# Performance work log

Hardware: AMD Instinct MI355X
Metric: run time of the kernel (lower is better)

## Reference

```python
import jax, jax.numpy as jnp
import numpy as np

WAVE_LEN = 1000.0

def rank_embedding(rank_dim, feat_dim):
    half = feat_dim // 2
    dim_mat = jnp.arange(half, dtype=jnp.float32) / half
    inv = 1.0 / jnp.power(WAVE_LEN, dim_mat)            # [half]
    mul = jnp.arange(rank_dim, dtype=jnp.float32)[:, None] * inv[None, :]  # [K, half]
    return jnp.concatenate([jnp.sin(mul), jnp.cos(mul)], axis=-1)          # [K, feat_dim]

def setup_inputs() -> dict:
    key = jax.random.key(0)
    ks = jax.random.split(key, 16)
    K, NS, NC, D, DF, H, DK = 2048, 18, 19, 1024, 128, 16, 64
    s = 0.02
    return {
        "size_scores": jax.random.normal(ks[0], (1, K, NS), jnp.float32),
        "size_residuals_normalized": jax.random.normal(ks[1], (1, K, NS, 3), jnp.float32),
        "sem_cls_scores": jax.random.normal(ks[2], (K, NC), jnp.float32),
        "appearance_features": jax.random.normal(ks[3], (K, D), jnp.float32),
        "mean_size_arr": jax.random.uniform(ks[4], (NS, 3), jnp.float32, 0.1, 1.0),
        "w_rank": jax.random.normal(ks[5], (D, DF), jnp.float32) * s,
        "b_rank": jnp.zeros((DF,), jnp.float32),
        "w_roi": jax.random.normal(ks[6], (D, DF), jnp.float32) * s,
        "b_roi": jnp.zeros((DF,), jnp.float32),
        "Wq": jax.random.normal(ks[7], (H, DF, DK), jnp.float32) * s,
        "Wk": jax.random.normal(ks[8], (H, DF, DK), jnp.float32) * s,
        "Wv": jax.random.normal(ks[9], (H, D, DK), jnp.float32) * s,
        "w_logit": jax.random.normal(ks[10], (D, 1), jnp.float32) * s,
        "b_logit": jnp.zeros((1,), jnp.float32),
    }

def reference(size_scores, size_residuals_normalized, sem_cls_scores,
              appearance_features, mean_size_arr,
              w_rank, b_rank, w_roi, b_roi, Wq, Wk, Wv, w_logit, b_logit):
    K, D = appearance_features.shape
    # --- predicted box size: gather residual for argmax size class ---
    pred_size_class = jnp.argmax(size_scores, axis=-1)                     # [1,K]
    size_residuals = size_residuals_normalized * mean_size_arr[None, None] # [1,K,NS,3]
    pred_size_residual = jnp.take_along_axis(
        size_residuals, pred_size_class[..., None, None], axis=2)[:, :, 0, :]  # [1,K,3]
    psc = pred_size_class[0]                                               # [K]
    box_size = mean_size_arr[psc] + pred_size_residual[0]                  # [K,3]
    # --- semantic class prob ---
    prob_all = jax.nn.softmax(sem_cls_scores, axis=-1)                     # [K,NC]
    prob = jnp.max(prob_all, axis=-1)                                      # [K]
    prob_argmax = jnp.argmax(prob_all, axis=-1)                            # [K]
    cls_bbox = box_size                                                    # [K,3]
    # --- background masking (jit-friendly analog of nonzero filtering):
    # background (class 0) proposals get key -1 so they sort to the end with score 0.
    fg = prob_argmax > 0
    sort_key = jnp.where(fg, prob, -1.0)
    order = jnp.argsort(-sort_key)                                         # descending
    sorted_prob = jnp.where(fg[order], prob[order], 0.0)                   # [K]
    sorted_labels = prob_argmax[order]                                     # [K]
    sorted_cls_bboxes = cls_bbox[order]                                    # [K,3]
    sorted_features = appearance_features[order]                           # [K,D]
    # --- rank embedding + roi embedding ---
    emb = rank_embedding(K, D)                                             # [K,D]
    nms_rank = emb @ w_rank + b_rank                                       # [K,DF]
    roi = sorted_features @ w_roi + b_roi                                  # [K,DF]
    e = nms_rank + roi                                                     # [K,DF]
    # --- relation-module self-attention: Q/K from embedding, V from features ---
    dk = Wq.shape[-1]
    q = jnp.einsum('kd,hde->hke', e, Wq)                                   # [H,K,dk]
    k = jnp.einsum('kd,hde->hke', e, Wk)
    scores = jnp.einsum('hke,hme->hkm', q, k) / jnp.sqrt(jnp.float32(dk))  # [H,K,K]
    attn = jax.nn.softmax(scores, axis=-1)
    v = jnp.einsum('kf,hfe->hke', sorted_features, Wv)                     # [H,K,dk]
    o = jnp.einsum('hkm,hme->hke', attn, v)                                # [H,K,dk]
    o = jnp.transpose(o, (1, 0, 2)).reshape(K, -1)                         # [K,D]
    attn_out = sorted_features + o                                         # residual
    # --- nms logit ---
    logit = attn_out @ w_logit + b_logit                                   # [K,1]
    s1 = jax.nn.sigmoid(logit).reshape(-1)
    nms_scores = s1 * sorted_prob
    return nms_scores, sorted_labels - 1, sorted_cls_bboxes
```

## Files before the change

kernel.cpp:

```cpp
#include <hip/hip_runtime.h>

#define KP 2048
#define DD 1024
#define DF 128
#define NH 16
#define DKK 64
#define NSS 18
#define NCC 19
#define NCH 4
#define CHUNK 512

typedef __attribute__((ext_vector_type(8))) short short8;
typedef __attribute__((ext_vector_type(4))) short short4_t;
typedef __attribute__((ext_vector_type(4))) float f32x4;

__device__ __forceinline__ short f2bf(float x){
    unsigned u = __float_as_uint(x);
    u += 0x7fffu + ((u >> 16) & 1u);
    return (short)(u >> 16);
}
__device__ __forceinline__ float bf2f(short s){
    return __uint_as_float(((unsigned)(unsigned short)s) << 16);
}

__device__ __forceinline__ void gl2lds16(const void* g, void* l){
    __builtin_amdgcn_global_load_lds((const __attribute__((address_space(1))) void*)g,
                                     (__attribute__((address_space(3))) void*)l, 16, 0, 0);
}

__global__ void prep_kernel(const float* __restrict__ size_scores,
                            const float* __restrict__ srn,
                            const float* __restrict__ sem,
                            const float* __restrict__ mean,
                            float* __restrict__ box, int* __restrict__ label,
                            double* __restrict__ probd, double* __restrict__ keyd){
    int k = blockIdx.x * blockDim.x + threadIdx.x;
    if (k >= KP) return;
    const float* ss = size_scores + k * NSS;
    int psc = 0; float bs = ss[0];
    for (int s = 1; s < NSS; s++){ float v = ss[s]; if (v > bs){ bs = v; psc = s; } }
    for (int c = 0; c < 3; c++){
        float m = mean[psc * 3 + c];
        float r = srn[k * (NSS * 3) + psc * 3 + c];
        box[k * 3 + c] = m + r * m;
    }
    const float* cs = sem + k * NCC;
    double mx = (double)cs[0]; int lab = 0;
    for (int c = 1; c < NCC; c++){ double v = (double)cs[c]; if (v > mx){ mx = v; lab = c; } }
    double sum = 0.0;
    for (int c = 0; c < NCC; c++) sum += exp((double)cs[c] - mx);
    double prob = 1.0 / sum;
    probd[k] = prob;
    label[k] = lab;
    keyd[k]  = (lab > 0) ? prob : -1.0;
}

__global__ __launch_bounds__(256) void rank_kernel(const double* __restrict__ keyd,
                                                   const int* __restrict__ label,
                                                   const double* __restrict__ probd,
                                                   const float* __restrict__ box,
                                                   int* __restrict__ order, float* __restrict__ sprob,
                                                   float* __restrict__ out){
    int i = blockIdx.x, t = threadIdx.x;
    double ki = keyd[i];
    const double2* k2 = (const double2*)keyd;
    int r = 0;
    #pragma unroll
    for (int p = 0; p < KP / 2 / 256; p++){
        int idx2 = p * 256 + t;
        double2 kj = k2[idx2];
        int j0 = idx2 * 2;
        r += (int)(kj.x > ki) + (int)((kj.x == ki) & (j0 < i));
        r += (int)(kj.y > ki) + (int)((kj.y == ki) & (j0 + 1 < i));
    }
    #pragma unroll
    for (int off = 32; off > 0; off >>= 1) r += __shfl_down(r, off);
    __shared__ int red[4];
    if ((t & 63) == 0) red[t >> 6] = r;
    __syncthreads();
    if (t == 0){
        int rk = red[0] + red[1] + red[2] + red[3];
        order[rk] = i;
        sprob[rk] = (label[i] > 0) ? (float)probd[i] : 0.f;
        out[KP + rk] = (float)(label[i] - 1);
        out[2 * KP + 3 * rk + 0] = box[i * 3 + 0];
        out[2 * KP + 3 * rk + 1] = box[i * 3 + 1];
        out[2 * KP + 3 * rk + 2] = box[i * 3 + 2];
    }
}

__global__ __launch_bounds__(256) void af_kernel(const float* __restrict__ app,
                                                 const int* __restrict__ order,
                                                 short* __restrict__ af){
    int pos = blockIdx.x, t = threadIdx.x;
    int ord = order[pos];
    float4 v = ((const float4*)(app + (size_t)ord * DD))[t];
    short4_t g = { f2bf(v.x), f2bf(v.y), f2bf(v.z), f2bf(v.w) };
    *(short4_t*)(af + (size_t)pos * 2048 + 1024 + t * 4) = g;
    short4_t e;
    #pragma unroll
    for (int i = 0; i < 4; i++){
        int j = t * 4 + i, jj = j & 511;
        float inv = exp2f(-(float)jj * 0.0194644224310197f);
        float arg = (float)pos * inv;
        e[i] = f2bf((j < 512) ? __sinf(arg) : __cosf(arg));
    }
    *(short4_t*)(af + (size_t)pos * 2048 + t * 4) = e;
}

__global__ __launch_bounds__(256) void convw_kernel(const float* __restrict__ w_rank,
                                                    const float* __restrict__ w_roi,
                                                    const float* __restrict__ Wq,
                                                    const float* __restrict__ Wk,
                                                    const float* __restrict__ Wv,
                                                    short* __restrict__ wcat,
                                                    short* __restrict__ qkT,
                                                    short* __restrict__ bvT){
    __shared__ float tile[64][65];
    int b = blockIdx.x;
    const float* src; short* dst; int sstride, dstride, r0, c0, doff;
    float scale = 1.0f;
    if (b < 32){        src = w_rank; dst = wcat; sstride = DF; dstride = 2048;
                        r0 = (b >> 1) * 64; c0 = (b & 1) * 64; doff = 0; }
    else if (b < 64){   int i = b - 32; src = w_roi; dst = wcat; sstride = DF; dstride = 2048;
                        r0 = (i >> 1) * 64; c0 = (i & 1) * 64; doff = 1024; }
    else if (b < 96){   int i = b - 64; int h = i >> 1;
                        src = Wq + (size_t)h * DF * DKK; dst = qkT + (size_t)h * DKK * DF;
                        sstride = DKK; dstride = DF; r0 = (i & 1) * 64; c0 = 0; doff = 0;
                        scale = 0.125f; }
    else if (b < 128){  int i = b - 96; int h = i >> 1;
                        src = Wk + (size_t)h * DF * DKK; dst = qkT + (size_t)(1024 + h * DKK) * DF;
                        sstride = DKK; dstride = DF; r0 = (i & 1) * 64; c0 = 0; doff = 0; }
    else {              int i = b - 128; int h = i >> 4;
                        src = Wv + (size_t)h * DD * DKK; dst = bvT + (size_t)h * DKK * DD;
                        sstride = DKK; dstride = DD; r0 = (i & 15) * 64; c0 = 0; doff = 0; }
    int tx = threadIdx.x & 63, ty = threadIdx.x >> 6;
    #pragma unroll
    for (int p = 0; p < 16; p++){
        int r = p * 4 + ty;
        tile[r][tx] = src[(size_t)(r0 + r) * sstride + c0 + tx];
    }
    __syncthreads();
    #pragma unroll
    for (int p = 0; p < 16; p++){
        int r = p * 4 + ty;
        dst[(size_t)(c0 + r) * dstride + doff + r0 + tx] = f2bf(tile[tx][r] * scale);
    }
}

__global__ __launch_bounds__(256) void gemm_lds(const short* __restrict__ A,
                                                const short* __restrict__ BT,
                                                void* __restrict__ C,
                                                int lda, int ldb, int N,
                                                int klen, size_t slabstride, int mode){
    int w = threadIdx.x >> 6, lane = threadIdx.x & 63;
    int quad = lane >> 4, l16 = lane & 15;
    int m0 = blockIdx.x * 64, n0 = blockIdx.y * 64;
    int kb = blockIdx.z * klen;

    __shared__ __align__(16) short alds[64 * 64];
    __shared__ __align__(16) short blds[64 * 64];

    int p0 = w * 64 + lane;
    int r0 = p0 >> 3, q0 = ((p0 & 7) ^ (r0 & 7)) * 8;
    int p1 = p0 + 256;
    int r1 = p1 >> 3, q1 = ((p1 & 7) ^ (r1 & 7)) * 8;
    short* adst0 = alds + w * 512;
    short* adst1 = alds + 2048 + w * 512;
    short* bdst0 = blds + w * 512;
    short* bdst1 = blds + 2048 + w * 512;
    const short* asrc0 = A + (size_t)(m0 + r0) * lda + kb + q0;
    const short* asrc1 = A + (size_t)(m0 + r1) * lda + kb + q1;
    const short* bsrc0 = BT + (size_t)(n0 + r0) * ldb + kb + q0;
    const short* bsrc1 = BT + (size_t)(n0 + r1) * ldb + kb + q1;

    f32x4 acc[4];
    for (int c = 0; c < 4; c++) acc[c] = (f32x4){0.f, 0.f, 0.f, 0.f};

    for (int kt = 0; kt < klen; kt += 64){
        __syncthreads();
        gl2lds16(asrc0 + kt, adst0);
        gl2lds16(asrc1 + kt, adst1);
        gl2lds16(bsrc0 + kt, bdst0);
        gl2lds16(bsrc1 + kt, bdst1);
        __syncthreads();
        int arow = w * 16 + l16;
        #pragma unroll
        for (int s = 0; s < 2; s++){
            short8 a = *(const short8*)(alds + arow * 64 + (((s * 4 + quad) ^ (l16 & 7)) * 8));
            #pragma unroll
            for (int c = 0; c < 4; c++){
                int brow = c * 16 + l16;
                short8 b = *(const short8*)(blds + brow * 64 + (((s * 4 + quad) ^ (l16 & 7)) * 8));
                acc[c] = __builtin_amdgcn_mfma_f32_16x16x32_bf16(a, b, acc[c], 0, 0, 0);
            }
        }
    }
    int mrow = m0 + w * 16 + quad * 4;
    #pragma unroll
    for (int c = 0; c < 4; c++){
        #pragma unroll
        for (int r = 0; r < 4; r++){
            size_t idx = (size_t)(mrow + r) * N + n0 + c * 16 + l16;
            if (mode == 2) ((short*)C)[idx] = f2bf(acc[c][r]);
            else ((float*)C + (size_t)blockIdx.z * slabstride)[idx] = acc[c][r];
        }
    }
}

__global__ __launch_bounds__(256) void combine_e_kernel(const float* __restrict__ es,
                                                        const float* __restrict__ b_rank,
                                                        const float* __restrict__ b_roi,
                                                        short* __restrict__ e_bf){
    int tid = blockIdx.x * 256 + threadIdx.x;
    int base = tid * 4;
    int n = base & (DF - 1);
    float4 s = *(const float4*)(es + base);
    #pragma unroll
    for (int c = 1; c < 4; c++){
        float4 t = *(const float4*)(es + (size_t)c * KP * DF + base);
        s.x += t.x; s.y += t.y; s.z += t.z; s.w += t.w;
    }
    float4 br = *(const float4*)(b_rank + n);
    float4 bo = *(const float4*)(b_roi + n);
    short4_t o = { f2bf(s.x + br.x + bo.x), f2bf(s.y + br.y + bo.y),
                   f2bf(s.z + br.z + bo.z), f2bf(s.w + br.w + bo.w) };
    *(short4_t*)(e_bf + base) = o;
}

__global__ __launch_bounds__(256, 4) void attn_kernel(const short* __restrict__ qk,
                                                      const short* __restrict__ vt_bf,
                                                      short* __restrict__ po,
                                                      float* __restrict__ pl){
    int qt = blockIdx.x, h = blockIdx.y, ch = blockIdx.z;
    int tid = threadIdx.x;
    int w = tid >> 6, lane = tid & 63, quad = lane >> 4, l16 = lane & 15;
    int qb = qt * 128;

    __shared__ __align__(16) short klds[64 * 64];
    __shared__ __align__(16) short vlds[64 * 64];
    __shared__ short plds[4][16 * 72];
    short* pw = plds[w];

    short8 aq[2][2];
    #pragma unroll
    for (int t = 0; t < 2; t++){
        const short* qrow = qk + (size_t)(qb + t * 64 + w * 16 + l16) * 2048 + h * DKK;
        aq[t][0] = *(const short8*)(qrow + quad * 8);
        aq[t][1] = *(const short8*)(qrow + 32 + quad * 8);
    }

    f32x4 oacc[2][4];
    float lpart[2][4];
    #pragma unroll
    for (int t = 0; t < 2; t++)
        #pragma unroll
        for (int c = 0; c < 4; c++){
            oacc[t][c] = (f32x4){0.f, 0.f, 0.f, 0.f};
            lpart[t][c] = 0.f;
        }

    int seg0 = w * 128 + lane;
    int row0 = seg0 >> 3, c80 = (seg0 & 7) ^ (row0 & 7);
    int seg1 = seg0 + 64;
    int row1 = seg1 >> 3, c81 = (seg1 & 7) ^ (row1 & 7);
    short* kl0 = klds + (size_t)(w * 128) * 8;
    short* kl1 = klds + (size_t)(w * 128 + 64) * 8;
    short* vl0 = vlds + (size_t)(w * 128) * 8;
    short* vl1 = vlds + (size_t)(w * 128 + 64) * 8;

    for (int m0 = ch * CHUNK; m0 < (ch + 1) * CHUNK; m0 += 64){
        __syncthreads();
        gl2lds16(qk + (size_t)(m0 + row0) * 2048 + 1024 + h * DKK + c80 * 8, kl0);
        gl2lds16(qk + (size_t)(m0 + row1) * 2048 + 1024 + h * DKK + c81 * 8, kl1);
        gl2lds16(vt_bf + (size_t)(h * DKK + row0) * KP + m0 + c80 * 8, vl0);
        gl2lds16(vt_bf + (size_t)(h * DKK + row1) * KP + m0 + c81 * 8, vl1);
        __syncthreads();

        #pragma unroll
        for (int t = 0; t < 2; t++){
            f32x4 s[4];
            #pragma unroll
            for (int c = 0; c < 4; c++){
                int r = c * 16 + l16, sw = r & 7;
                short8 b0 = *(const short8*)(klds + r * 64 + (quad ^ sw) * 8);
                short8 b1 = *(const short8*)(klds + r * 64 + ((quad + 4) ^ sw) * 8);
                f32x4 acc = (f32x4){0.f, 0.f, 0.f, 0.f};
                acc = __builtin_amdgcn_mfma_f32_16x16x32_bf16(aq[t][0], b0, acc, 0, 0, 0);
                acc = __builtin_amdgcn_mfma_f32_16x16x32_bf16(aq[t][1], b1, acc, 0, 0, 0);
                #pragma unroll
                for (int rr = 0; rr < 4; rr++) s[c][rr] = __expf(acc[rr]);
            }
            #pragma unroll
            for (int c = 0; c < 4; c++)
                #pragma unroll
                for (int rr = 0; rr < 4; rr++){
                    lpart[t][rr] += s[c][rr];
                    pw[(quad * 4 + rr) * 72 + c * 16 + l16] = f2bf(s[c][rr]);
                }
            short8 pa0 = *(const short8*)(pw + l16 * 72 + quad * 8);
            short8 pa1 = *(const short8*)(pw + l16 * 72 + 32 + quad * 8);
            #pragma unroll
            for (int c = 0; c < 4; c++){
                int r = c * 16 + l16, sw = r & 7;
                short8 bv0 = *(const short8*)(vlds + r * 64 + (quad ^ sw) * 8);
                short8 bv1 = *(const short8*)(vlds + r * 64 + ((quad + 4) ^ sw) * 8);
                oacc[t][c] = __builtin_amdgcn_mfma_f32_16x16x32_bf16(pa0, bv0, oacc[t][c], 0, 0, 0);
                oacc[t][c] = __builtin_amdgcn_mfma_f32_16x16x32_bf16(pa1, bv1, oacc[t][c], 0, 0, 0);
            }
        }
    }

    #pragma unroll
    for (int t = 0; t < 2; t++){
        #pragma unroll
        for (int rr = 0; rr < 4; rr++){
            float v = lpart[t][rr];
            v += __shfl_xor(v, 1); v += __shfl_xor(v, 2);
            v += __shfl_xor(v, 4); v += __shfl_xor(v, 8);
            lpart[t][rr] = v;
        }
        int qr0 = qb + t * 64 + w * 16;
        if (l16 == 0){
            #pragma unroll
            for (int rr = 0; rr < 4; rr++)
                pl[((size_t)ch * NH + h) * KP + qr0 + quad * 4 + rr] = lpart[t][rr];
        }
        #pragma unroll
        for (int c = 0; c < 4; c++)
            #pragma unroll
            for (int rr = 0; rr < 4; rr++)
                po[(size_t)ch * KP * DD + (size_t)(qr0 + quad * 4 + rr) * DD + h * DKK + c * 16 + l16]
                    = f2bf(oacc[t][c][rr]);
    }
}

__global__ __launch_bounds__(256) void final_kernel(const float* __restrict__ app,
                                                    const int* __restrict__ order,
                                                    const short* __restrict__ po,
                                                    const float* __restrict__ pl,
                                                    const float* __restrict__ w_logit,
                                                    const float* __restrict__ b_logit,
                                                    const float* __restrict__ sprob,
                                                    float* __restrict__ out){
    int pos = blockIdx.x, t = threadIdx.x;
    int ord = order[pos];
    int d = t * 4;
    int h = d >> 6;
    float l = 0.f;
    #pragma unroll
    for (int c = 0; c < NCH; c++) l += pl[((size_t)c * NH + h) * KP + pos];
    float inv = 1.f / l;
    float sx = 0, sy = 0, sz = 0, sw = 0;
    #pragma unroll
    for (int c = 0; c < NCH; c++){
        short4_t p = *(const short4_t*)(po + (size_t)c * KP * DD + (size_t)pos * DD + d);
        sx += bf2f(p[0]); sy += bf2f(p[1]); sz += bf2f(p[2]); sw += bf2f(p[3]);
    }
    float4 a = *(const float4*)(app + (size_t)ord * DD + d);
    float4 wv = *(const float4*)(w_logit + d);
    float partial = (a.x + sx * inv) * wv.x + (a.y + sy * inv) * wv.y +
                    (a.z + sz * inv) * wv.z + (a.w + sw * inv) * wv.w;
    for (int off = 32; off > 0; off >>= 1) partial += __shfl_down(partial, off);
    __shared__ float red[4];
    if ((t & 63) == 0) red[t >> 6] = partial;
    __syncthreads();
    if (t == 0){
        float logit = red[0] + red[1] + red[2] + red[3] + b_logit[0];
        float s1 = 1.f / (1.f + __expf(-logit));
        out[pos] = s1 * sprob[pos];
    }
}

extern "C" void kernel_launch(void* const* d_in, const int* in_sizes, int n_in,
                              void* d_out, int out_size, void* d_ws, size_t ws_size,
                              hipStream_t stream){
    (void)in_sizes; (void)n_in; (void)out_size; (void)ws_size;
    const float* size_scores = (const float*)d_in[0];
    const float* srn     = (const float*)d_in[1];
    const float* sem     = (const float*)d_in[2];
    const float* app     = (const float*)d_in[3];
    const float* mean    = (const float*)d_in[4];
    const float* w_rank  = (const float*)d_in[5];
    const float* b_rank  = (const float*)d_in[6];
    const float* w_roi   = (const float*)d_in[7];
    const float* b_roi   = (const float*)d_in[8];
    const float* Wq      = (const float*)d_in[9];
    const float* Wk      = (const float*)d_in[10];
    const float* Wv      = (const float*)d_in[11];
    const float* w_logit = (const float*)d_in[12];
    const float* b_logit = (const float*)d_in[13];
    float* out = (float*)d_out;

    char* ws = (char*)d_ws;
    size_t off = 0;
    auto alloc = [&](size_t n) -> char* {
        char* p = ws + off;
        off = (off + n + 255) & ~(size_t)255;
        return p;
    };
    float*  box    = (float*) alloc((size_t)KP * 3 * 4);
    int*    label  = (int*)   alloc((size_t)KP * 4);
    double* probd  = (double*)alloc((size_t)KP * 8);
    double* keyd   = (double*)alloc((size_t)KP * 8);
    int*    order  = (int*)   alloc((size_t)KP * 4);
    float*  sprob  = (float*) alloc((size_t)KP * 4);
    short*  wcat   = (short*) alloc((size_t)DF * 2048 * 2);
    short*  qkT    = (short*) alloc((size_t)2048 * DF * 2);
    short*  bvT    = (short*) alloc((size_t)DD * DD * 2);
    short*  e_bf   = (short*) alloc((size_t)KP * DF * 2);
    short*  qk_bf  = (short*) alloc((size_t)KP * 2048 * 2);
    short*  vt_bf  = (short*) alloc((size_t)DD * KP * 2);
    float*  pl     = (float*) alloc((size_t)NCH * NH * KP * 4);
    char*   X      = alloc((size_t)NCH * KP * DD * 2);
    short*  af     = (short*)X;
    float*  es     = (float*)(X + (size_t)8 * 1024 * 1024);
    short*  po     = (short*)X;

    prep_kernel<<<KP / 256, 256, 0, stream>>>(size_scores, srn, sem, mean, box, label, probd, keyd);
    rank_kernel<<<KP, 256, 0, stream>>>(keyd, label, probd, box, order, sprob, out);
    af_kernel<<<KP, 256, 0, stream>>>(app, order, af);
    convw_kernel<<<384, 256, 0, stream>>>(w_rank, w_roi, Wq, Wk, Wv, wcat, qkT, bvT);
    gemm_lds<<<dim3(KP / 64, DF / 64, 4), 256, 0, stream>>>(af, wcat, es, 2048, 2048, DF, 512,
                                                            (size_t)KP * DF, 0);
    combine_e_kernel<<<(KP * DF / 4) / 256, 256, 0, stream>>>(es, b_rank, b_roi, e_bf);
    gemm_lds<<<dim3(KP / 64, 2048 / 64, 1), 256, 0, stream>>>(e_bf, qkT, qk_bf, DF, DF, 2048, DF,
                                                              0, 2);
    gemm_lds<<<dim3(DD / 64, KP / 64, 1), 256, 0, stream>>>(bvT, af + 1024, vt_bf, DD, 2048, KP, DD,
                                                            0, 2);
    attn_kernel<<<dim3(KP / 128, NH, NCH), 256, 0, stream>>>(qk_bf, vt_bf, po, pl);
    final_kernel<<<KP, 256, 0, stream>>>(app, order, po, pl, w_logit, b_logit, sprob, out);
}
```

Baseline: 170.6 us.

## Fold logit projection into V so attention reduces to weighted scalar sums

Only the logit (attn_out @ w_logit) is consumed downstream, so w_logit is folded into Wv per head to give a 1024x16 projection. The per-key scalar values are then computed with a small MFMA kernel. Attention now accumulates only exp-sums and exp-weighted scalar sums instead of the full PV MFMA with a 64-wide V tile. This drops the large V GEMM, the V LDS staging, the bf16 partial-output writes and their readback in the final kernel, at the cost of slight numeric reordering and bf16 rounding of the folded weights.

```diff
diff --git a/kernel.cpp b/kernel.cpp
--- a/kernel.cpp
+++ b/kernel.cpp
@@ -18,9 +18,6 @@
     unsigned u = __float_as_uint(x);
     u += 0x7fffu + ((u >> 16) & 1u);
     return (short)(u >> 16);
-}
-__device__ __forceinline__ float bf2f(short s){
-    return __uint_as_float(((unsigned)(unsigned short)s) << 16);
 }
 
 __device__ __forceinline__ void gl2lds16(const void* g, void* l){
@@ -113,11 +110,24 @@
                                                     const float* __restrict__ Wq,
                                                     const float* __restrict__ Wk,
                                                     const float* __restrict__ Wv,
+                                                    const float* __restrict__ w_logit,
                                                     short* __restrict__ wcat,
                                                     short* __restrict__ qkT,
-                                                    short* __restrict__ bvT){
+                                                    short* __restrict__ uT){
+    int b = blockIdx.x;
+    if (b >= 128){
+        int i = b - 128;
+        int h = i >> 2;
+        int f = ((i & 3) << 8) + threadIdx.x;
+        const float* wv = Wv + (size_t)h * DD * DKK + (size_t)f * DKK;
+        const float* wlh = w_logit + h * DKK;
+        float s = 0.f;
+        #pragma unroll
+        for (int e = 0; e < DKK; e++) s += wv[e] * wlh[e];
+        uT[h * DD + f] = f2bf(s);
+        return;
+    }
     __shared__ float tile[64][65];
-    int b = blockIdx.x;
     const float* src; short* dst; int sstride, dstride, r0, c0, doff;
     float scale = 1.0f;
     if (b < 32){        src = w_rank; dst = wcat; sstride = DF; dstride = 2048;
@@ -128,12 +138,9 @@
                         src = Wq + (size_t)h * DF * DKK; dst = qkT + (size_t)h * DKK * DF;
                         sstride = DKK; dstride = DF; r0 = (i & 1) * 64; c0 = 0; doff = 0;
                         scale = 0.125f; }
-    else if (b < 128){  int i = b - 96; int h = i >> 1;
+    else {              int i = b - 96; int h = i >> 1;
                         src = Wk + (size_t)h * DF * DKK; dst = qkT + (size_t)(1024 + h * DKK) * DF;
                         sstride = DKK; dstride = DF; r0 = (i & 1) * 64; c0 = 0; doff = 0; }
-    else {              int i = b - 128; int h = i >> 4;
-                        src = Wv + (size_t)h * DD * DKK; dst = bvT + (size_t)h * DKK * DD;
-                        sstride = DKK; dstride = DD; r0 = (i & 15) * 64; c0 = 0; doff = 0; }
     int tx = threadIdx.x & 63, ty = threadIdx.x >> 6;
     #pragma unroll
     for (int p = 0; p < 16; p++){
@@ -228,19 +235,35 @@
     *(short4_t*)(e_bf + base) = o;
 }
 
+__global__ __launch_bounds__(256) void vw_kernel(const short* __restrict__ af,
+                                                 const short* __restrict__ uT,
+                                                 float* __restrict__ vwT){
+    int w = threadIdx.x >> 6, lane = threadIdx.x & 63;
+    int quad = lane >> 4, l16 = lane & 15;
+    int m0 = blockIdx.x * 64 + w * 16;
+    f32x4 acc = (f32x4){0.f, 0.f, 0.f, 0.f};
+    const short* arow = af + (size_t)(m0 + l16) * 2048 + 1024 + quad * 8;
+    const short* brow = uT + (size_t)l16 * DD + quad * 8;
+    for (int k0 = 0; k0 < DD; k0 += 32){
+        short8 a = *(const short8*)(arow + k0);
+        short8 b = *(const short8*)(brow + k0);
+        acc = __builtin_amdgcn_mfma_f32_16x16x32_bf16(a, b, acc, 0, 0, 0);
+    }
+    #pragma unroll
+    for (int r = 0; r < 4; r++)
+        vwT[(size_t)l16 * KP + m0 + quad * 4 + r] = acc[r];
+}
+
 __global__ __launch_bounds__(256, 4) void attn_kernel(const short* __restrict__ qk,
-                                                      const short* __restrict__ vt_bf,
-                                                      short* __restrict__ po,
-                                                      float* __restrict__ pl){
+                                                      const float* __restrict__ vwT,
+                                                      float* __restrict__ pl,
+                                                      float* __restrict__ pwl){
     int qt = blockIdx.x, h = blockIdx.y, ch = blockIdx.z;
     int tid = threadIdx.x;
     int w = tid >> 6, lane = tid & 63, quad = lane >> 4, l16 = lane & 15;
     int qb = qt * 128;
 
     __shared__ __align__(16) short klds[64 * 64];
-    __shared__ __align__(16) short vlds[64 * 64];
-    __shared__ short plds[4][16 * 72];
-    short* pw = plds[w];
 
     short8 aq[2][2];
     #pragma unroll
@@ -250,15 +273,8 @@
         aq[t][1] = *(const short8*)(qrow + 32 + quad * 8);
     }
 
-    f32x4 oacc[2][4];
-    float lpart[2][4];
-    #pragma unroll
-    for (int t = 0; t < 2; t++)
-        #pragma unroll
-        for (int c = 0; c < 4; c++){
-            oacc[t][c] = (f32x4){0.f, 0.f, 0.f, 0.f};
-            lpart[t][c] = 0.f;
-        }
+    float lpart[2][4] = {{0.f,0.f,0.f,0.f},{0.f,0.f,0.f,0.f}};
+    float wpart[2][4] = {{0.f,0.f,0.f,0.f},{0.f,0.f,0.f,0.f}};
 
     int seg0 = w * 128 + lane;
     int row0 = seg0 >> 3, c80 = (seg0 & 7) ^ (row0 & 7);
@@ -266,20 +282,19 @@
     int row1 = seg1 >> 3, c81 = (seg1 & 7) ^ (row1 & 7);
     short* kl0 = klds + (size_t)(w * 128) * 8;
     short* kl1 = klds + (size_t)(w * 128 + 64) * 8;
-    short* vl0 = vlds + (size_t)(w * 128) * 8;
-    short* vl1 = vlds + (size_t)(w * 128 + 64) * 8;
 
     for (int m0 = ch * CHUNK; m0 < (ch + 1) * CHUNK; m0 += 64){
         __syncthreads();
         gl2lds16(qk + (size_t)(m0 + row0) * 2048 + 1024 + h * DKK + c80 * 8, kl0);
         gl2lds16(qk + (size_t)(m0 + row1) * 2048 + 1024 + h * DKK + c81 * 8, kl1);
-        gl2lds16(vt_bf + (size_t)(h * DKK + row0) * KP + m0 + c80 * 8, vl0);
-        gl2lds16(vt_bf + (size_t)(h * DKK + row1) * KP + m0 + c81 * 8, vl1);
+        float vwv[4];
+        #pragma unroll
+        for (int c = 0; c < 4; c++)
+            vwv[c] = vwT[(size_t)h * KP + m0 + c * 16 + l16];
         __syncthreads();
 
         #pragma unroll
         for (int t = 0; t < 2; t++){
-            f32x4 s[4];
             #pragma unroll
             for (int c = 0; c < 4; c++){
                 int r = c * 16 + l16, sw = r & 7;
@@ -289,84 +304,69 @@
                 acc = __builtin_amdgcn_mfma_f32_16x16x32_bf16(aq[t][0], b0, acc, 0, 0, 0);
                 acc = __builtin_amdgcn_mfma_f32_16x16x32_bf16(aq[t][1], b1, acc, 0, 0, 0);
                 #pragma unroll
-                for (int rr = 0; rr < 4; rr++) s[c][rr] = __expf(acc[rr]);
+                for (int rr = 0; rr < 4; rr++){
+                    float e = __expf(acc[rr]);
+                    lpart[t][rr] += e;
+                    wpart[t][rr] += e * vwv[c];
+                }
             }
+        }
+    }
+
+    #pragma unroll
+    for (int t = 0; t < 2; t++){
+        #pragma unroll
+        for (int rr = 0; rr < 4; rr++){
+            float v = lpart[t][rr], x = wpart[t][rr];
+            v += __shfl_xor(v, 1); x += __shfl_xor(x, 1);
+            v += __shfl_xor(v, 2); x += __shfl_xor(x, 2);
+            v += __shfl_xor(v, 4); x += __shfl_xor(x, 4);
+            v += __shfl_xor(v, 8); x += __shfl_xor(x, 8);
+            lpart[t][rr] = v; wpart[t][rr] = x;
+        }
+        if (l16 == 0){
+            int qr0 = qb + t * 64 + w * 16;
             #pragma unroll
-            for (int c = 0; c < 4; c++)
-                #pragma unroll
-                for (int rr = 0; rr < 4; rr++){
-                    lpart[t][rr] += s[c][rr];
-                    pw[(quad * 4 + rr) * 72 + c * 16 + l16] = f2bf(s[c][rr]);
-                }
-            short8 pa0 = *(const short8*)(pw + l16 * 72 + quad * 8);
-            short8 pa1 = *(const short8*)(pw + l16 * 72 + 32 + quad * 8);
-            #pragma unroll
-            for (int c = 0; c < 4; c++){
-                int r = c * 16 + l16, sw = r & 7;
-                short8 bv0 = *(const short8*)(vlds + r * 64 + (quad ^ sw) * 8);
-                short8 bv1 = *(const short8*)(vlds + r * 64 + ((quad + 4) ^ sw) * 8);
-                oacc[t][c] = __builtin_amdgcn_mfma_f32_16x16x32_bf16(pa0, bv0, oacc[t][c], 0, 0, 0);
-                oacc[t][c] = __builtin_amdgcn_mfma_f32_16x16x32_bf16(pa1, bv1, oacc[t][c], 0, 0, 0);
+            for (int rr = 0; rr < 4; rr++){
+                size_t idx = ((size_t)ch * NH + h) * KP + qr0 + quad * 4 + rr;
+                pl[idx]  = lpart[t][rr];
+                pwl[idx] = wpart[t][rr];
             }
         }
-    }
-
-    #pragma unroll
-    for (int t = 0; t < 2; t++){
-        #pragma unroll
-        for (int rr = 0; rr < 4; rr++){
-            float v = lpart[t][rr];
-            v += __shfl_xor(v, 1); v += __shfl_xor(v, 2);
-            v += __shfl_xor(v, 4); v += __shfl_xor(v, 8);
-            lpart[t][rr] = v;
-        }
-        int qr0 = qb + t * 64 + w * 16;
-        if (l16 == 0){
-            #pragma unroll
-            for (int rr = 0; rr < 4; rr++)
-                pl[((size_t)ch * NH + h) * KP + qr0 + quad * 4 + rr] = lpart[t][rr];
-        }
-        #pragma unroll
-        for (int c = 0; c < 4; c++)
-            #pragma unroll
-            for (int rr = 0; rr < 4; rr++)
-                po[(size_t)ch * KP * DD + (size_t)(qr0 + quad * 4 + rr) * DD + h * DKK + c * 16 + l16]
-                    = f2bf(oacc[t][c][rr]);
     }
 }
 
 __global__ __launch_bounds__(256) void final_kernel(const float* __restrict__ app,
                                                     const int* __restrict__ order,
-                                                    const short* __restrict__ po,
                                                     const float* __restrict__ pl,
+                                                    const float* __restrict__ pwl,
                                                     const float* __restrict__ w_logit,
                                                     const float* __restrict__ b_logit,
                                                     const float* __restrict__ sprob,
                                                     float* __restrict__ out){
     int pos = blockIdx.x, t = threadIdx.x;
     int ord = order[pos];
-    int d = t * 4;
-    int h = d >> 6;
-    float l = 0.f;
-    #pragma unroll
-    for (int c = 0; c < NCH; c++) l += pl[((size_t)c * NH + h) * KP + pos];
-    float inv = 1.f / l;
-    float sx = 0, sy = 0, sz = 0, sw = 0;
-    #pragma unroll
-    for (int c = 0; c < NCH; c++){
-        short4_t p = *(const short4_t*)(po + (size_t)c * KP * DD + (size_t)pos * DD + d);
-        sx += bf2f(p[0]); sy += bf2f(p[1]); sz += bf2f(p[2]); sw += bf2f(p[3]);
-    }
-    float4 a = *(const float4*)(app + (size_t)ord * DD + d);
-    float4 wv = *(const float4*)(w_logit + d);
-    float partial = (a.x + sx * inv) * wv.x + (a.y + sy * inv) * wv.y +
-                    (a.z + sz * inv) * wv.z + (a.w + sw * inv) * wv.w;
+    float4 a = *(const float4*)(app + (size_t)ord * DD + t * 4);
+    float4 wv = *(const float4*)(w_logit + t * 4);
+    float partial = a.x * wv.x + a.y * wv.y + a.z * wv.z + a.w * wv.w;
     for (int off = 32; off > 0; off >>= 1) partial += __shfl_down(partial, off);
     __shared__ float red[4];
+    __shared__ float hsum[NH];
     if ((t & 63) == 0) red[t >> 6] = partial;
+    if (t < NH){
+        float l = 0.f, x = 0.f;
+        #pragma unroll
+        for (int c = 0; c < NCH; c++){
+            size_t idx = ((size_t)c * NH + t) * KP + pos;
+            l += pl[idx]; x += pwl[idx];
+        }
+        hsum[t] = x / l;
+    }
     __syncthreads();
     if (t == 0){
         float logit = red[0] + red[1] + red[2] + red[3] + b_logit[0];
+        #pragma unroll
+        for (int h = 0; h < NH; h++) logit += hsum[h];
         float s1 = 1.f / (1.f + __expf(-logit));
         out[pos] = s1 * sprob[pos];
     }
@@ -407,27 +407,26 @@
     float*  sprob  = (float*) alloc((size_t)KP * 4);
     short*  wcat   = (short*) alloc((size_t)DF * 2048 * 2);
     short*  qkT    = (short*) alloc((size_t)2048 * DF * 2);
-    short*  bvT    = (short*) alloc((size_t)DD * DD * 2);
+    short*  uT     = (short*) alloc((size_t)NH * DD * 2);
     short*  e_bf   = (short*) alloc((size_t)KP * DF * 2);
     short*  qk_bf  = (short*) alloc((size_t)KP * 2048 * 2);
-    short*  vt_bf  = (short*) alloc((size_t)DD * KP * 2);
+    float*  vwT    = (float*) alloc((size_t)NH * KP * 4);
     float*  pl     = (float*) alloc((size_t)NCH * NH * KP * 4);
-    char*   X      = alloc((size_t)NCH * KP * DD * 2);
+    float*  pwl    = (float*) alloc((size_t)NCH * NH * KP * 4);
+    char*   X      = alloc((size_t)12 * 1024 * 1024);
     short*  af     = (short*)X;
     float*  es     = (float*)(X + (size_t)8 * 1024 * 1024);
-    short*  po     = (short*)X;
 
     prep_kernel<<<KP / 256, 256, 0, stream>>>(size_scores, srn, sem, mean, box, label, probd, keyd);
     rank_kernel<<<KP, 256, 0, stream>>>(keyd, label, probd, box, order, sprob, out);
     af_kernel<<<KP, 256, 0, stream>>>(app, order, af);
-    convw_kernel<<<384, 256, 0, stream>>>(w_rank, w_roi, Wq, Wk, Wv, wcat, qkT, bvT);
+    convw_kernel<<<192, 256, 0, stream>>>(w_rank, w_roi, Wq, Wk, Wv, w_logit, wcat, qkT, uT);
     gemm_lds<<<dim3(KP / 64, DF / 64, 4), 256, 0, stream>>>(af, wcat, es, 2048, 2048, DF, 512,
                                                             (size_t)KP * DF, 0);
     combine_e_kernel<<<(KP * DF / 4) / 256, 256, 0, stream>>>(es, b_rank, b_roi, e_bf);
     gemm_lds<<<dim3(KP / 64, 2048 / 64, 1), 256, 0, stream>>>(e_bf, qkT, qk_bf, DF, DF, 2048, DF,
                                                               0, 2);
-    gemm_lds<<<dim3(DD / 64, KP / 64, 1), 256, 0, stream>>>(bvT, af + 1024, vt_bf, DD, 2048, KP, DD,
-                                                            0, 2);
-    attn_kernel<<<dim3(KP / 128, NH, NCH), 256, 0, stream>>>(qk_bf, vt_bf, po, pl);
-    final_kernel<<<KP, 256, 0, stream>>>(app, order, po, pl, w_logit, b_logit, sprob, out);
-}
+    vw_kernel<<<KP / 64, 256, 0, stream>>>(af, uT, vwT);
+    attn_kernel<<<dim3(KP / 128, NH, NCH), 256, 0, stream>>>(qk_bf, vwT, pl, pwl);
+    final_kernel<<<KP, 256, 0, stream>>>(app, order, pl, pwl, w_logit, b_logit, sprob, out);
+}
```

Result: faster. 150.5 us (-11.8%).
